# Kernel tuning notes

Hardware: AMD Instinct MI355X
Metric: run time of the kernel (lower is better)

## Reference

```python
import jax, jax.numpy as jnp
import numpy as np

D_MODEL = 1024
N_HEADS = 16
D_FF = 4 * D_MODEL
CTX = 2048
EPS = 1e-5


def setup_inputs() -> dict:
    key = jax.random.key(0)
    ks = jax.random.split(key, 8)
    s = 0.02
    z = jax.random.normal(ks[0], (2, CTX, D_MODEL), dtype=jnp.float32)
    W_Q = jax.random.normal(ks[1], (D_MODEL, D_MODEL), dtype=jnp.float32) * s
    W_K = jax.random.normal(ks[2], (D_MODEL, D_MODEL), dtype=jnp.float32) * s
    W_V = jax.random.normal(ks[3], (D_MODEL, D_MODEL), dtype=jnp.float32) * s
    W_O = jax.random.normal(ks[4], (D_MODEL, D_MODEL), dtype=jnp.float32) * s
    W_fc = jax.random.normal(ks[5], (D_MODEL, D_FF), dtype=jnp.float32) * s
    W_proj = jax.random.normal(ks[6], (D_FF, D_MODEL), dtype=jnp.float32) * s
    g1 = jnp.ones((D_MODEL,), dtype=jnp.float32)
    g2 = jnp.ones((D_MODEL,), dtype=jnp.float32)
    return {"z": z, "W_Q": W_Q, "W_K": W_K, "W_V": W_V, "W_O": W_O,
            "W_fc": W_fc, "W_proj": W_proj, "g1": g1, "g2": g2}


def rmsnorm(x, gain):
    rms = jnp.sqrt(jnp.sum(x * x, axis=-1, keepdims=True) / x.shape[-1] + EPS)
    return (x / rms) * gain


def gelu_erf(x):
    return x * 0.5 * (1.0 + jax.lax.erf(x / jnp.sqrt(2.0).astype(x.dtype)))


def attention(zn, W_Q, W_K, W_V, W_O):
    B, T, D = zn.shape
    H = N_HEADS
    dh = D // H
    # [B,T,D] -> [B,H,T,dh]
    def split(x):
        return x.reshape(B, T, H, dh).transpose(0, 2, 1, 3)
    Q = split(zn @ W_Q)
    K = split(zn @ W_K)
    V = split(zn @ W_V)
    scores = jnp.einsum('bhtd,bhsd->bhts', Q, K) / jnp.sqrt(jnp.float32(dh))
    causal = jnp.triu(jnp.ones((T, T), dtype=bool), k=1)  # True above diagonal -> masked
    scores = jnp.where(causal[None, None], -jnp.inf, scores)
    weights = jax.nn.softmax(scores, axis=-1)
    ctx = jnp.einsum('bhts,bhsd->bhtd', weights, V)
    ctx = ctx.transpose(0, 2, 1, 3).reshape(B, T, D)
    return ctx @ W_O


def reference(z, W_Q, W_K, W_V, W_O, W_fc, W_proj, g1, g2):
    # pre-norm GPT block: z + attn(norm1(z)); then + ffn(norm2(z))
    z = z + attention(rmsnorm(z, g1), W_Q, W_K, W_V, W_O)
    h = rmsnorm(z, g2)
    ffn = gelu_erf(h @ W_fc) @ W_proj
    return z + ffn
```

## Files before the change

kernel.cpp:

```cpp
#include <hip/hip_runtime.h>
#include <hip/hip_bf16.h>
#include <math.h>


typedef __bf16 bf16x8 __attribute__((ext_vector_type(8)));
typedef float  f32x4  __attribute__((ext_vector_type(4)));

#define MFMA_16x16x32_BF16(A, B, C) __builtin_amdgcn_mfma_f32_16x16x32_bf16((A), (B), (C), 0, 0, 0)

#define GLDS16(g, l) __builtin_amdgcn_global_load_lds( \
    (const __attribute__((address_space(1))) void*)(g), \
    (__attribute__((address_space(3))) void*)(l), 16, 0, 0)

__global__ __launch_bounds__(256) void transconv_all_kernel(
    const float* __restrict__ W_Q, const float* __restrict__ W_K,
    const float* __restrict__ W_V, const float* __restrict__ W_O,
    const float* __restrict__ W_fc, const float* __restrict__ W_proj,
    __bf16* __restrict__ WtQKV, __bf16* __restrict__ WtO,
    __bf16* __restrict__ Wtfc, __bf16* __restrict__ Wtproj)
{
    const int id = blockIdx.x;
    const float* src;
    __bf16* dst;
    int K, N, nx, t;
    if (id < 4096) {
        const int wsel = id >> 10;
        t = id & 1023;
        src = (wsel == 0) ? W_Q : (wsel == 1) ? W_K : (wsel == 2) ? W_V : W_O;
        dst = (wsel < 3) ? (WtQKV + (size_t)wsel * 1048576) : WtO;
        K = 1024; N = 1024; nx = 32;
    } else if (id < 8192) {
        t = id - 4096; src = W_fc; dst = Wtfc; K = 1024; N = 4096; nx = 128;
    } else {
        t = id - 8192; src = W_proj; dst = Wtproj; K = 4096; N = 1024; nx = 32;
    }
    const int n0 = (t % nx) * 32, k0 = (t / nx) * 32;

    __shared__ float tile[32][33];
    const int c = threadIdx.x & 31, r = threadIdx.x >> 5;
#pragma unroll
    for (int i = 0; i < 4; ++i)
        tile[r + 8 * i][c] = src[(size_t)(k0 + r + 8 * i) * N + n0 + c];
    __syncthreads();
#pragma unroll
    for (int i = 0; i < 4; ++i)
        dst[(size_t)(n0 + r + 8 * i) * K + k0 + c] = (__bf16)tile[c][r + 8 * i];
}

__global__ __launch_bounds__(256) void rmsnorm_kernel(
    const float* __restrict__ x, const float* __restrict__ gain,
    __bf16* __restrict__ out)
{
    const int row = blockIdx.x, t = threadIdx.x;
    const float4 v = ((const float4*)(x + (size_t)row * 1024))[t];
    float ss = v.x * v.x + v.y * v.y + v.z * v.z + v.w * v.w;
#pragma unroll
    for (int m = 1; m < 64; m <<= 1) ss += __shfl_xor(ss, m);
    __shared__ float red[4];
    const int wid = t >> 6, lane = t & 63;
    if (lane == 0) red[wid] = ss;
    __syncthreads();
    const float tot = red[0] + red[1] + red[2] + red[3];
    const float inv = rsqrtf(tot * (1.0f / 1024.0f) + 1e-5f);
    const float4 gv = ((const float4*)gain)[t];
    __bf16* o = out + (size_t)row * 1024 + t * 4;
    o[0] = (__bf16)(v.x * inv * gv.x);
    o[1] = (__bf16)(v.y * inv * gv.y);
    o[2] = (__bf16)(v.z * inv * gv.z);
    o[3] = (__bf16)(v.w * inv * gv.w);
}

template <int BM, int BN, int EPI>
__global__ __launch_bounds__(256) void gemm_bf16(
    const __bf16* __restrict__ A, const __bf16* __restrict__ Bt,
    void* __restrict__ outp, const float* __restrict__ res,
    int M, int N, int K)
{
    __shared__ __bf16 As[2][BM * 64];
    __shared__ __bf16 Bs[2][BN * 64];
    const int tid = threadIdx.x;

    const int gx = gridDim.x, nwg = gx * gridDim.y;
    int bid = blockIdx.y * gx + blockIdx.x;
    if ((nwg & 7) == 0) bid = (bid & 7) * (nwg >> 3) + (bid >> 3);
    const int m0 = (bid / gx) * BM, n0 = (bid % gx) * BN;

    const int lane = tid & 63, w = tid >> 6;
    const int wm = w >> 1, wn = w & 1;
    const int lr = lane & 15, g = lane >> 4;
    const int srow = lane >> 3;
    const int scol = ((lane & 7) ^ srow) * 8;
    const int xr8 = lr & 7;

    constexpr int MI = BM / 32, NI = BN / 32;
    f32x4 acc[MI][NI] = {};

    const __bf16* Abase = A + (size_t)m0 * K;
    const __bf16* Bbase = Bt + (size_t)n0 * K;

    auto STAGE = [&](int kb, int buf) {
#pragma unroll
        for (int j = 0; j < BM / 32; ++j) {
            const int s = j * 4 + w;
            GLDS16(Abase + (size_t)(s * 8 + srow) * K + kb + scol, &As[buf][s * 512]);
        }
#pragma unroll
        for (int j = 0; j < BN / 32; ++j) {
            const int s = j * 4 + w;
            GLDS16(Bbase + (size_t)(s * 8 + srow) * K + kb + scol, &Bs[buf][s * 512]);
        }
    };

    const int nt = K >> 6;
    STAGE(0, 0);
    __syncthreads();

    for (int t = 0; t < nt; ++t) {
        const int cur = t & 1;
        if (t + 1 < nt) STAGE((t + 1) << 6, cur ^ 1);

        bf16x8 af[2][MI], bfr[2][NI];
#pragma unroll
        for (int kk = 0; kk < 2; ++kk) {
#pragma unroll
            for (int i = 0; i < MI; ++i)
                af[kk][i] = *(const bf16x8*)
                    &As[cur][(wm * (BM / 2) + i * 16 + lr) * 64 + (((kk * 4 + g) ^ xr8) << 3)];
#pragma unroll
            for (int i = 0; i < NI; ++i)
                bfr[kk][i] = *(const bf16x8*)
                    &Bs[cur][(wn * (BN / 2) + i * 16 + lr) * 64 + (((kk * 4 + g) ^ xr8) << 3)];
        }
#pragma unroll
        for (int kk = 0; kk < 2; ++kk)
#pragma unroll
            for (int mi = 0; mi < MI; ++mi)
#pragma unroll
                for (int ni = 0; ni < NI; ++ni)
                    acc[mi][ni] = MFMA_16x16x32_BF16(af[kk][mi], bfr[kk][ni], acc[mi][ni]);
        if (t + 1 < nt) __syncthreads();
    }

#pragma unroll
    for (int mi = 0; mi < MI; ++mi)
#pragma unroll
        for (int ni = 0; ni < NI; ++ni) {
            const int colg = n0 + wn * (BN / 2) + ni * 16 + lr;
#pragma unroll
            for (int r = 0; r < 4; ++r) {
                const int rowg = m0 + wm * (BM / 2) + mi * 16 + 4 * g + r;
                const float v = acc[mi][ni][r];
                if constexpr (EPI == 1) {
                    const size_t idx = (size_t)rowg * N + colg;
                    ((float*)outp)[idx] = res[idx] + v;
                } else if constexpr (EPI == 2) {
                    const size_t idx = (size_t)rowg * N + colg;
                    ((__bf16*)outp)[idx] =
                        (__bf16)(0.5f * v * (1.0f + erff(v * 0.70710678118654752f)));
                } else if constexpr (EPI == 3) {
                    const size_t idx = (size_t)rowg * N + colg;
                    ((float*)outp)[idx] += v;
                } else {
                    __bf16* base = (__bf16*)outp;
                    const int seg = colg >> 10;
                    const int cg = colg & 1023;
                    if (seg < 2) {
                        base[(size_t)seg * 4194304 + (size_t)rowg * 1024 + cg] = (__bf16)v;
                    } else {
                        const int tt = rowg & 2047;
                        const int r32 = tt & 31;
                        const int p = ((r32 & 12) << 1) | ((r32 >> 2) & 4) | (r32 & 3);
                        base[8388608 +
                             ((size_t)((rowg >> 11) * 16 + (cg >> 6)) * 64 + (cg & 63)) * 2048 +
                             ((tt & ~31) | p)] = (__bf16)v;
                    }
                }
            }
        }
}

__global__ __launch_bounds__(256) void attn_kernel(
    const __bf16* __restrict__ Q, const __bf16* __restrict__ Kb,
    const __bf16* __restrict__ Vt, __bf16* __restrict__ ctx)
{
    const int Dm = 1024, T = 2048;
    const int tid = threadIdx.x;
    const int w = tid >> 6, lane = tid & 63;
    const int lr = lane & 15, g = lane >> 4;
    const int bx = blockIdx.x;
    const int qc = bx >> 5, bh = bx & 31, b = bh >> 4, h = bh & 15;
    const int qbase = qc * 64 + w * 16;
    const size_t rowoff = (size_t)b * T;
    const __bf16* Qp = Q + rowoff * Dm + h * 64;
    const __bf16* Kp = Kb + rowoff * Dm + h * 64;
    const __bf16* Vtp = Vt + (size_t)bh * 64 * 2048;

    __shared__ __bf16 Ks[2][64 * 64];
    __shared__ __bf16 Vs[2][64 * 64];

    bf16x8 qf0 = *(const bf16x8*)&Qp[(size_t)(qbase + lr) * Dm + g * 8];
    bf16x8 qf1 = *(const bf16x8*)&Qp[(size_t)(qbase + lr) * Dm + 32 + g * 8];
#pragma unroll
    for (int j = 0; j < 8; ++j) {
        qf0[j] = (__bf16)((float)qf0[j] * 0.125f);
        qf1[j] = (__bf16)((float)qf1[j] * 0.125f);
    }

    const int srow = lane >> 3;
    const int schunk = (lane & 7) ^ srow;

    f32x4 acc[4] = {};
    float m_s = -__builtin_inff(), l_s = 0.0f;
    const int nsteps = qc + 1;
    const f32x4 zacc = {0.0f, 0.0f, 0.0f, 0.0f};
    const int xr = (lr & 7) << 3;
    const int qg = qbase + lr;

#pragma unroll
    for (int j = 0; j < 2; ++j) {
        const int row = j * 32 + w * 8 + srow;
        GLDS16(Kp + (size_t)row * Dm + schunk * 8, &Ks[0][(j * 32 + w * 8) * 64]);
        GLDS16(Vtp + (size_t)row * T + schunk * 8, &Vs[0][(j * 32 + w * 8) * 64]);
    }
    __syncthreads();

    for (int t = 0; t < nsteps; ++t) {
        const int kvb = t * 64, cur = t & 1;
        if (t + 1 < nsteps) {
#pragma unroll
            for (int j = 0; j < 2; ++j) {
                const int row = j * 32 + w * 8 + srow;
                GLDS16(Kp + (size_t)(kvb + 64 + row) * Dm + schunk * 8,
                       &Ks[cur ^ 1][(j * 32 + w * 8) * 64]);
                GLDS16(Vtp + (size_t)row * T + kvb + 64 + schunk * 8,
                       &Vs[cur ^ 1][(j * 32 + w * 8) * 64]);
            }
        }

        float sv[4][4];
#pragma unroll
        for (int s4 = 0; s4 < 4; ++s4) {
            const int kv0 = kvb + s4 * 16;
            if (kv0 <= qbase + 15) {
                const int row = s4 * 16 + lr;
                const bf16x8 kfa = *(const bf16x8*)&Ks[cur][row * 64 + ((g * 8) ^ xr)];
                const bf16x8 kfb = *(const bf16x8*)&Ks[cur][row * 64 + ((32 + g * 8) ^ xr)];
                f32x4 st = MFMA_16x16x32_BF16(kfa, qf0, zacc);
                st = MFMA_16x16x32_BF16(kfb, qf1, st);
                const bool domask = (kv0 + 15 > qbase);
#pragma unroll
                for (int r = 0; r < 4; ++r) {
                    float x = st[r];
                    if (domask && (kv0 + 4 * g + r > qg)) x = -__builtin_inff();
                    sv[s4][r] = x;
                }
            } else {
#pragma unroll
                for (int r = 0; r < 4; ++r) sv[s4][r] = -__builtin_inff();
            }
        }

        float tm = sv[0][0];
#pragma unroll
        for (int s4 = 0; s4 < 4; ++s4)
#pragma unroll
            for (int r = 0; r < 4; ++r) tm = fmaxf(tm, sv[s4][r]);
        tm = fmaxf(tm, __shfl_xor(tm, 16));
        tm = fmaxf(tm, __shfl_xor(tm, 32));

        float m_use = m_s;
        if (!__all(tm - m_s <= 8.0f)) {
            m_use = fmaxf(m_s, tm);
            const float corr = __expf(m_s - m_use);
            l_s *= corr;
            float cr[4];
#pragma unroll
            for (int r = 0; r < 4; ++r) cr[r] = __shfl(corr, 4 * g + r);
#pragma unroll
            for (int ct = 0; ct < 4; ++ct) {
                acc[ct][0] *= cr[0]; acc[ct][1] *= cr[1];
                acc[ct][2] *= cr[2]; acc[ct][3] *= cr[3];
            }
            m_s = m_use;
        }

        float rs = 0.0f;
#pragma unroll
        for (int s4 = 0; s4 < 4; ++s4)
#pragma unroll
            for (int r = 0; r < 4; ++r) {
                sv[s4][r] = __expf(sv[s4][r] - m_use);
                rs += sv[s4][r];
            }
        rs += __shfl_xor(rs, 16);
        rs += __shfl_xor(rs, 32);
        l_s += rs;

        bf16x8 pa0, pa1;
#pragma unroll
        for (int r = 0; r < 4; ++r) {
            pa0[r] = (__bf16)sv[0][r];
            pa0[4 + r] = (__bf16)sv[1][r];
            pa1[r] = (__bf16)sv[2][r];
            pa1[4 + r] = (__bf16)sv[3][r];
        }
        const bool liveB = (kvb + 32 <= qbase + 15);
#pragma unroll
        for (int ct = 0; ct < 4; ++ct) {
            const __bf16* vrow = &Vs[cur][(ct * 16 + lr) * 64];
            const bf16x8 vf = *(const bf16x8*)&vrow[(8 * g) ^ xr];
            acc[ct] = MFMA_16x16x32_BF16(pa0, vf, acc[ct]);
            if (liveB) {
                const bf16x8 vf2 = *(const bf16x8*)&vrow[(32 + 8 * g) ^ xr];
                acc[ct] = MFMA_16x16x32_BF16(pa1, vf2, acc[ct]);
            }
        }
        __syncthreads();
    }

    float dn[4];
#pragma unroll
    for (int r = 0; r < 4; ++r) dn[r] = __shfl(l_s, 4 * g + r);
#pragma unroll
    for (int ct = 0; ct < 4; ++ct)
#pragma unroll
        for (int r = 0; r < 4; ++r)
            ctx[(rowoff + qbase + 4 * g + r) * Dm + h * 64 + ct * 16 + lr] =
                (__bf16)(acc[ct][r] / dn[r]);
}

extern "C" void kernel_launch(void* const* d_in, const int* in_sizes, int n_in,
                              void* d_out, int out_size, void* d_ws, size_t ws_size,
                              hipStream_t stream)
{
    (void)in_sizes; (void)n_in; (void)out_size; (void)ws_size;
    const float* z      = (const float*)d_in[0];
    const float* W_Q    = (const float*)d_in[1];
    const float* W_K    = (const float*)d_in[2];
    const float* W_V    = (const float*)d_in[3];
    const float* W_O    = (const float*)d_in[4];
    const float* W_fc   = (const float*)d_in[5];
    const float* W_proj = (const float*)d_in[6];
    const float* g1     = (const float*)d_in[7];
    const float* g2     = (const float*)d_in[8];
    float* out = (float*)d_out;

    char* ws = (char*)d_ws;
    const size_t MB = (size_t)1 << 20;
    __bf16* WtQKV  = (__bf16*)(ws + 0 * MB);
    __bf16* WtO    = (__bf16*)(ws + 6 * MB);
    __bf16* Wtfc   = (__bf16*)(ws + 8 * MB);
    __bf16* Wtproj = (__bf16*)(ws + 16 * MB);
    __bf16* zn     = (__bf16*)(ws + 24 * MB);
    __bf16* Qb     = (__bf16*)(ws + 32 * MB);
    __bf16* Kbuf   = (__bf16*)(ws + 40 * MB);
    __bf16* Vtb    = (__bf16*)(ws + 48 * MB);
    __bf16* ffn1   = (__bf16*)(ws + 40 * MB);
    __bf16* ctx    = zn;
    __bf16* hb     = Qb;

    const int Tt = 2048, Dm = 1024, Bb = 2, M = Bb * Tt, DFF = 4096;
    const dim3 blk256(256);

    transconv_all_kernel<<<12288, blk256, 0, stream>>>(
        W_Q, W_K, W_V, W_O, W_fc, W_proj, WtQKV, WtO, Wtfc, Wtproj);

    rmsnorm_kernel<<<M, blk256, 0, stream>>>(z, g1, zn);

    gemm_bf16<128, 128, 4><<<dim3(24, 32), blk256, 0, stream>>>(
        zn, WtQKV, Qb, nullptr, M, 3072, Dm);

    attn_kernel<<<1024, blk256, 0, stream>>>(Qb, Kbuf, Vtb, ctx);

    gemm_bf16<128, 64, 1><<<dim3(16, 32), blk256, 0, stream>>>(
        ctx, WtO, out, z, M, Dm, Dm);

    rmsnorm_kernel<<<M, blk256, 0, stream>>>(out, g2, hb);

    gemm_bf16<128, 128, 2><<<dim3(32, 32), blk256, 0, stream>>>(
        hb, Wtfc, ffn1, nullptr, M, DFF, Dm);

    gemm_bf16<128, 64, 3><<<dim3(16, 32), blk256, 0, stream>>>(
        ffn1, Wtproj, out, nullptr, M, Dm, DFF);
}
```

Measured before the change: 275.6 us.

## Add 256x256 ping-pong GEMM for QKV/FC and use exp2 softmax in attention

Adds a new 512-thread GEMM kernel with 256x256 tiles, double-buffered LDS halves, explicit barrier-interleaved staging and raised wave priority around MFMA blocks. The QKV and FC projections now use it, which cuts global traffic per FLOP and gives more MFMA work per barrier. Attention now folds log2(e) into the Q scale and uses exp2f, a wider rescale threshold, a reciprocal multiply for normalization, and setprio around PV MFMAs. Larger tiles give fewer workgroups (192 and 256), which may leave some of the 256 CUs underused, and the looser threshold changes the numeric headroom of the softmax.

```diff
diff --git a/kernel.cpp b/kernel.cpp
--- a/kernel.cpp
+++ b/kernel.cpp
@@ -70,6 +70,156 @@
     o[3] = (__bf16)(v.w * inv * gv.w);
 }
 
+template <int EPI>
+__device__ __forceinline__ void epi_write(
+    void* outp, const float* res, int N, int rowg, int colg, float v)
+{
+    if constexpr (EPI == 1) {
+        const size_t idx = (size_t)rowg * N + colg;
+        ((float*)outp)[idx] = res[idx] + v;
+    } else if constexpr (EPI == 2) {
+        const size_t idx = (size_t)rowg * N + colg;
+        ((__bf16*)outp)[idx] =
+            (__bf16)(0.5f * v * (1.0f + erff(v * 0.70710678118654752f)));
+    } else if constexpr (EPI == 3) {
+        const size_t idx = (size_t)rowg * N + colg;
+        ((float*)outp)[idx] += v;
+    } else {
+        __bf16* base = (__bf16*)outp;
+        const int seg = colg >> 10;
+        const int cg = colg & 1023;
+        if (seg < 2) {
+            base[(size_t)seg * 4194304 + (size_t)rowg * 1024 + cg] = (__bf16)v;
+        } else {
+            const int tt = rowg & 2047;
+            const int r32 = tt & 31;
+            const int p = ((r32 & 12) << 1) | ((r32 >> 2) & 4) | (r32 & 3);
+            base[8388608 +
+                 ((size_t)((rowg >> 11) * 16 + (cg >> 6)) * 64 + (cg & 63)) * 2048 +
+                 ((tt & ~31) | p)] = (__bf16)v;
+        }
+    }
+}
+
+template <int EPI>
+__global__ __launch_bounds__(512, 2) void gemm256(
+    const __bf16* __restrict__ A, const __bf16* __restrict__ Bt,
+    void* __restrict__ outp, const float* __restrict__ res,
+    int M, int N, int K)
+{
+    __shared__ __bf16 As[2][2][128 * 64];
+    __shared__ __bf16 Bs[2][2][128 * 64];
+    const int tid = threadIdx.x;
+
+    const int gx = gridDim.x, nwg = gx * gridDim.y;
+    int bid = blockIdx.y * gx + blockIdx.x;
+    if ((nwg & 7) == 0) bid = (bid & 7) * (nwg >> 3) + (bid >> 3);
+    const int m0 = (bid / gx) * 256, n0 = (bid % gx) * 256;
+
+    const int lane = tid & 63, w = tid >> 6;
+    const int wr = w >> 2, wc = w & 3;
+    const int lr = lane & 15, g = lane >> 4;
+    const int srow8 = lane >> 3, schunk = (lane & 7) ^ srow8;
+    const int xk = lr & 7;
+    const int wch = wc >> 1, bro = (wc & 1) * 64;
+
+    const __bf16* Ab = A + (size_t)m0 * K;
+    const __bf16* Bb = Bt + (size_t)n0 * K;
+
+    auto STG = [&](const __bf16* gb, __bf16* lds, int kt, int half) {
+        const __bf16* src = gb + (size_t)(half * 128) * K + (kt << 6);
+#pragma unroll
+        for (int j = 0; j < 2; ++j) {
+            const int sidx = j * 8 + w;
+            GLDS16(src + (size_t)(sidx * 8 + srow8) * K + schunk * 8, lds + sidx * 512);
+        }
+    };
+
+    f32x4 acc[8][4] = {};
+    bf16x8 af[2][4], bf[2][4];
+
+#define LAF(BUF, QM) do {                                                       \
+    _Pragma("unroll") for (int i_ = 0; i_ < 4; ++i_)                            \
+    _Pragma("unroll") for (int kk_ = 0; kk_ < 2; ++kk_)                         \
+        af[kk_][i_] = *(const bf16x8*)&As[BUF][wr]                              \
+            [((QM) * 64 + i_ * 16 + lr) * 64 + (((kk_ * 4 + g) ^ xk) << 3)];    \
+    } while (0)
+
+#define LBF(BUF, QN) do {                                                       \
+    _Pragma("unroll") for (int i_ = 0; i_ < 2; ++i_)                            \
+    _Pragma("unroll") for (int kk_ = 0; kk_ < 2; ++kk_)                         \
+        bf[kk_][(QN) * 2 + i_] = *(const bf16x8*)&Bs[BUF][wch]                  \
+            [(bro + ((QN) * 2 + i_) * 16 + lr) * 64 + (((kk_ * 4 + g) ^ xk) << 3)]; \
+    } while (0)
+
+#define MMQ(QM, QN) do {                                                        \
+    __builtin_amdgcn_s_setprio(1);                                              \
+    _Pragma("unroll") for (int kk_ = 0; kk_ < 2; ++kk_)                         \
+    _Pragma("unroll") for (int i_ = 0; i_ < 4; ++i_)                            \
+    _Pragma("unroll") for (int n_ = 0; n_ < 2; ++n_)                            \
+        acc[(QM) * 4 + i_][(QN) * 2 + n_] = MFMA_16x16x32_BF16(                 \
+            af[kk_][i_], bf[kk_][(QN) * 2 + n_], acc[(QM) * 4 + i_][(QN) * 2 + n_]); \
+    __builtin_amdgcn_s_setprio(0);                                              \
+    } while (0)
+
+#define BAR()  __builtin_amdgcn_s_barrier()
+#define VMC(N_) asm volatile("s_waitcnt vmcnt(" #N_ ")" ::: "memory")
+#define SGB0() __builtin_amdgcn_sched_barrier(0)
+
+    const int nt = K >> 6, niter = nt >> 1;
+
+    STG(Ab, &As[0][0][0], 0, 0); STG(Ab, &As[0][1][0], 0, 1);
+    STG(Bb, &Bs[0][0][0], 0, 0); STG(Bb, &Bs[0][1][0], 0, 1);
+    STG(Bb, &Bs[1][0][0], 1, 0); STG(Bb, &Bs[1][1][0], 1, 1);
+
+    for (int i = 0; i < niter - 1; ++i) {
+        const int t1 = 2 * i + 1;
+        STG(Ab, &As[1][0][0], t1, 0);
+        VMC(6); BAR(); SGB0();
+        LAF(0, 0); LBF(0, 0); MMQ(0, 0); BAR();
+        LBF(0, 1); STG(Ab, &As[1][1][0], t1, 1); BAR(); MMQ(0, 1); BAR();
+        LAF(0, 1); STG(Bb, &Bs[0][0][0], t1 + 1, 0); BAR(); MMQ(1, 0); BAR();
+        STG(Bb, &Bs[0][1][0], t1 + 1, 1); BAR(); MMQ(1, 1); BAR();
+        STG(Ab, &As[0][0][0], t1 + 1, 0);
+        VMC(6); BAR(); SGB0();
+        LAF(1, 0); LBF(1, 0); MMQ(0, 0); BAR();
+        LBF(1, 1); STG(Ab, &As[0][1][0], t1 + 1, 1); BAR(); MMQ(0, 1); BAR();
+        LAF(1, 1); STG(Bb, &Bs[1][0][0], t1 + 2, 0); BAR(); MMQ(1, 0); BAR();
+        STG(Bb, &Bs[1][1][0], t1 + 2, 1); BAR(); MMQ(1, 1); BAR();
+    }
+    {
+        STG(Ab, &As[1][0][0], nt - 1, 0);
+        VMC(6); BAR(); SGB0();
+        LAF(0, 0); LBF(0, 0); MMQ(0, 0); BAR();
+        LBF(0, 1); STG(Ab, &As[1][1][0], nt - 1, 1); BAR(); MMQ(0, 1); BAR();
+        LAF(0, 1); BAR(); MMQ(1, 0); BAR();
+        BAR(); MMQ(1, 1); BAR();
+        VMC(0); BAR(); SGB0();
+        LAF(1, 0); LBF(1, 0); MMQ(0, 0); BAR();
+        LBF(1, 1); BAR(); MMQ(0, 1); BAR();
+        LAF(1, 1); BAR(); MMQ(1, 0); BAR();
+        BAR(); MMQ(1, 1); BAR();
+    }
+#undef LAF
+#undef LBF
+#undef MMQ
+#undef BAR
+#undef VMC
+#undef SGB0
+
+#pragma unroll
+    for (int mi = 0; mi < 8; ++mi)
+#pragma unroll
+        for (int ni = 0; ni < 4; ++ni) {
+            const int colg = n0 + wc * 64 + ni * 16 + lr;
+#pragma unroll
+            for (int r = 0; r < 4; ++r) {
+                const int rowg = m0 + wr * 128 + mi * 16 + 4 * g + r;
+                epi_write<EPI>(outp, res, N, rowg, colg, acc[mi][ni][r]);
+            }
+        }
+}
+
 template <int BM, int BN, int EPI>
 __global__ __launch_bounds__(256) void gemm_bf16(
     const __bf16* __restrict__ A, const __bf16* __restrict__ Bt,
@@ -149,32 +299,7 @@
 #pragma unroll
             for (int r = 0; r < 4; ++r) {
                 const int rowg = m0 + wm * (BM / 2) + mi * 16 + 4 * g + r;
-                const float v = acc[mi][ni][r];
-                if constexpr (EPI == 1) {
-                    const size_t idx = (size_t)rowg * N + colg;
-                    ((float*)outp)[idx] = res[idx] + v;
-                } else if constexpr (EPI == 2) {
-                    const size_t idx = (size_t)rowg * N + colg;
-                    ((__bf16*)outp)[idx] =
-                        (__bf16)(0.5f * v * (1.0f + erff(v * 0.70710678118654752f)));
-                } else if constexpr (EPI == 3) {
-                    const size_t idx = (size_t)rowg * N + colg;
-                    ((float*)outp)[idx] += v;
-                } else {
-                    __bf16* base = (__bf16*)outp;
-                    const int seg = colg >> 10;
-                    const int cg = colg & 1023;
-                    if (seg < 2) {
-                        base[(size_t)seg * 4194304 + (size_t)rowg * 1024 + cg] = (__bf16)v;
-                    } else {
-                        const int tt = rowg & 2047;
-                        const int r32 = tt & 31;
-                        const int p = ((r32 & 12) << 1) | ((r32 >> 2) & 4) | (r32 & 3);
-                        base[8388608 +
-                             ((size_t)((rowg >> 11) * 16 + (cg >> 6)) * 64 + (cg & 63)) * 2048 +
-                             ((tt & ~31) | p)] = (__bf16)v;
-                    }
-                }
+                epi_write<EPI>(outp, res, N, rowg, colg, acc[mi][ni][r]);
             }
         }
 }
@@ -200,10 +325,11 @@
 
     bf16x8 qf0 = *(const bf16x8*)&Qp[(size_t)(qbase + lr) * Dm + g * 8];
     bf16x8 qf1 = *(const bf16x8*)&Qp[(size_t)(qbase + lr) * Dm + 32 + g * 8];
+    const float qsc = 0.125f * 1.44269504088896340736f;
 #pragma unroll
     for (int j = 0; j < 8; ++j) {
-        qf0[j] = (__bf16)((float)qf0[j] * 0.125f);
-        qf1[j] = (__bf16)((float)qf1[j] * 0.125f);
+        qf0[j] = (__bf16)((float)qf0[j] * qsc);
+        qf1[j] = (__bf16)((float)qf1[j] * qsc);
     }
 
     const int srow = lane >> 3;
@@ -269,9 +395,9 @@
         tm = fmaxf(tm, __shfl_xor(tm, 32));
 
         float m_use = m_s;
-        if (!__all(tm - m_s <= 8.0f)) {
+        if (!__all(tm - m_s <= 11.5f)) {
             m_use = fmaxf(m_s, tm);
-            const float corr = __expf(m_s - m_use);
+            const float corr = exp2f(m_s - m_use);
             l_s *= corr;
             float cr[4];
 #pragma unroll
@@ -289,7 +415,7 @@
         for (int s4 = 0; s4 < 4; ++s4)
 #pragma unroll
             for (int r = 0; r < 4; ++r) {
-                sv[s4][r] = __expf(sv[s4][r] - m_use);
+                sv[s4][r] = exp2f(sv[s4][r] - m_use);
                 rs += sv[s4][r];
             }
         rs += __shfl_xor(rs, 16);
@@ -305,6 +431,7 @@
             pa1[4 + r] = (__bf16)sv[3][r];
         }
         const bool liveB = (kvb + 32 <= qbase + 15);
+        __builtin_amdgcn_s_setprio(1);
 #pragma unroll
         for (int ct = 0; ct < 4; ++ct) {
             const __bf16* vrow = &Vs[cur][(ct * 16 + lr) * 64];
@@ -315,18 +442,20 @@
                 acc[ct] = MFMA_16x16x32_BF16(pa1, vf2, acc[ct]);
             }
         }
+        __builtin_amdgcn_s_setprio(0);
         __syncthreads();
     }
 
+    const float il = __builtin_amdgcn_rcpf(l_s);
     float dn[4];
 #pragma unroll
-    for (int r = 0; r < 4; ++r) dn[r] = __shfl(l_s, 4 * g + r);
+    for (int r = 0; r < 4; ++r) dn[r] = __shfl(il, 4 * g + r);
 #pragma unroll
     for (int ct = 0; ct < 4; ++ct)
 #pragma unroll
         for (int r = 0; r < 4; ++r)
             ctx[(rowoff + qbase + 4 * g + r) * Dm + h * 64 + ct * 16 + lr] =
-                (__bf16)(acc[ct][r] / dn[r]);
+                (__bf16)(acc[ct][r] * dn[r]);
 }
 
 extern "C" void kernel_launch(void* const* d_in, const int* in_sizes, int n_in,
@@ -360,14 +489,14 @@
     __bf16* hb     = Qb;
 
     const int Tt = 2048, Dm = 1024, Bb = 2, M = Bb * Tt, DFF = 4096;
-    const dim3 blk256(256);
+    const dim3 blk256(256), blk512(512);
 
     transconv_all_kernel<<<12288, blk256, 0, stream>>>(
         W_Q, W_K, W_V, W_O, W_fc, W_proj, WtQKV, WtO, Wtfc, Wtproj);
 
     rmsnorm_kernel<<<M, blk256, 0, stream>>>(z, g1, zn);
 
-    gemm_bf16<128, 128, 4><<<dim3(24, 32), blk256, 0, stream>>>(
+    gemm256<4><<<dim3(12, 16), blk512, 0, stream>>>(
         zn, WtQKV, Qb, nullptr, M, 3072, Dm);
 
     attn_kernel<<<1024, blk256, 0, stream>>>(Qb, Kbuf, Vtb, ctx);
@@ -377,7 +506,7 @@
 
     rmsnorm_kernel<<<M, blk256, 0, stream>>>(out, g2, hb);
 
-    gemm_bf16<128, 128, 2><<<dim3(32, 32), blk256, 0, stream>>>(
+    gemm256<2><<<dim3(16, 16), blk512, 0, stream>>>(
         hb, Wtfc, ffn1, nullptr, M, DFF, Dm);
 
     gemm_bf16<128, 64, 3><<<dim3(16, 32), blk256, 0, stream>>>(
```

New measurement: 290.6 us. 1.05x slower.
